# Performance work log

Measured on AMD Instinct MI355X. Metric: run time of the kernel, lower is better.

Reference implementation:

```python
import jax, jax.numpy as jnp
import numpy as np

INV_TEMP = 10.0

def pairwise_distance(x, y):
    # squared L2 distance: [b,n,c],[b,m,c] -> [b,n,m]
    x2 = jnp.sum(x * x, axis=-1, keepdims=True)          # [b,n,1]
    y2 = jnp.sum(y * y, axis=-1)[:, None, :]             # [b,1,m]
    xy = jnp.einsum('bnc,bmc->bnm', x, y)                # [b,n,m]
    return x2 + y2 - 2.0 * xy

def setup_inputs() -> dict:
    key = jax.random.key(0)
    k1, k2, k3 = jax.random.split(key, 3)
    b, n, m, c = 4, 4096, 4096, 32
    x_f = jax.random.normal(k1, (b, n, c), dtype=jnp.float32)
    y_f = jax.random.normal(k2, (b, m, c), dtype=jnp.float32)
    y_c = jax.random.normal(k3, (b, m, 3), dtype=jnp.float32)
    temp_inv = jnp.ones((1,), dtype=jnp.float32) * INV_TEMP
    return {"x_f": x_f, "y_f": y_f, "y_c": y_c, "temp_inv": temp_inv}

def reference(x_f, y_f, y_c, temp_inv):
    # corr_type='soft', st=True (straight-through)
    dist = pairwise_distance(x_f, y_f)                   # [b,n,m]
    y_soft = jax.nn.softmax(-dist * temp_inv[0], axis=2) # [b,n,m]
    index = jnp.argmax(y_soft, axis=2)                   # [b,n]
    y_hard = jax.nn.one_hot(index, y_soft.shape[2], dtype=y_soft.dtype)
    ret = y_hard - jax.lax.stop_gradient(y_soft) + y_soft
    x_corr = jnp.matmul(ret, y_c)                        # [b,n,3]
    return x_corr
```

## Files before the change

kernel.cpp:

```cpp
#include <hip/hip_runtime.h>

#define B 4
#define N 4096
#define M 4096
#define C 32
#define BN (B * N)
#define MS 16

typedef short bf16x8 __attribute__((ext_vector_type(8)));
typedef float f32x4  __attribute__((ext_vector_type(4)));
typedef unsigned int u32x4 __attribute__((ext_vector_type(4)));

#define WS_WI ((size_t)MS * BN * 4)
#define WS_YH (WS_WI * 2)
#define WS_YM (WS_YH + (size_t)B * M * C * 2)
#define WS_YL (WS_YM + (size_t)B * M * C * 2)
#define WS_Y2 (WS_YL + (size_t)B * M * C * 2)

__device__ __forceinline__ float bf16lo(unsigned int u) { return __uint_as_float(u << 16); }
__device__ __forceinline__ float bf16hi(unsigned int u) { return __uint_as_float(u & 0xffff0000u); }

__device__ __forceinline__ void split3(const float f[8], bf16x8& h, bf16x8& m, bf16x8& l) {
    u32x4 hw, mw, lw;
    #pragma unroll
    for (int p = 0; p < 4; ++p) {
        const float f0 = f[2*p], f1 = f[2*p+1];
        const unsigned int h0 = __float_as_uint(f0) & 0xffff0000u;
        const unsigned int h1 = __float_as_uint(f1) & 0xffff0000u;
        hw[p] = h1 | (h0 >> 16);
        const float r0 = f0 - __uint_as_float(h0);
        const float r1 = f1 - __uint_as_float(h1);
        const unsigned int m0 = __float_as_uint(r0) & 0xffff0000u;
        const unsigned int m1 = __float_as_uint(r1) & 0xffff0000u;
        mw[p] = m1 | (m0 >> 16);
        const float s0 = r0 - __uint_as_float(m0);
        const float s1 = r1 - __uint_as_float(m1);
        lw[p] = (__float_as_uint(s1) & 0xffff0000u) | (__float_as_uint(s0) >> 16);
    }
    h = __builtin_bit_cast(bf16x8, hw);
    m = __builtin_bit_cast(bf16x8, mw);
    l = __builtin_bit_cast(bf16x8, lw);
}

__global__ __launch_bounds__(256)
void y_prepass(const void* __restrict__ yptr, const unsigned short* __restrict__ tptr,
               void* __restrict__ ws) {
    if (tptr[0] == 0x4120) return;
    unsigned short* yh = (unsigned short*)((char*)ws + WS_YH);
    unsigned short* ym = (unsigned short*)((char*)ws + WS_YM);
    unsigned short* yl = (unsigned short*)((char*)ws + WS_YL);
    float*          y2 = (float*)((char*)ws + WS_Y2);

    const int gid = blockIdx.x * 256 + threadIdx.x;
    const int row = gid >> 2;
    const int seg = gid & 3;
    const float* p = (const float*)yptr + (size_t)row * C + seg * 8;
    float4 v0 = *(const float4*)p;
    float4 v1 = *(const float4*)(p + 4);
    const float f[8] = {v0.x, v0.y, v0.z, v0.w, v1.x, v1.y, v1.z, v1.w};

    bf16x8 h, m, l;
    split3(f, h, m, l);
    const size_t o = (size_t)row * C + seg * 8;
    *(bf16x8*)(yh + o) = h;
    *(bf16x8*)(ym + o) = m;
    *(bf16x8*)(yl + o) = l;

    float s = 0.f;
    #pragma unroll
    for (int k = 0; k < 8; ++k) s = fmaf(f[k], f[k], s);
    s += __shfl_xor(s, 1, 64);
    s += __shfl_xor(s, 2, 64);
    if (seg == 0) y2[row] = -0.5f * s;
}

__global__ __launch_bounds__(256, 4)
void nn_main(const void* __restrict__ xptr, const void* __restrict__ yptr,
             const unsigned short* __restrict__ tptr, void* __restrict__ ws) {
    float* wD = (float*)ws;
    int*   wI = (int*)((char*)ws + WS_WI);
    const bool is_bf16 = (tptr[0] == 0x4120);

    __shared__ float y2s[256];

    const int tid  = threadIdx.x;
    const int lane = tid & 63;
    const int wv   = tid >> 6;
    const int col  = lane & 15;
    const int quad = lane >> 4;
    const int bi   = blockIdx.x;
    const int ms   = bi & 15;
    const int nb   = (bi >> 4) & 31;
    const int b    = bi >> 9;
    const int n_base = nb * 128 + wv * 32;
    const int m0   = ms * 256;

    float bD[2][4];
    int   bI[2][4];
    #pragma unroll
    for (int t = 0; t < 2; ++t)
        #pragma unroll
        for (int r = 0; r < 4; ++r) { bD[t][r] = -__builtin_inff(); bI[t][r] = 0; }

    const size_t boff = (size_t)col * C + quad * 8;

    if (is_bf16) {
        const unsigned short* yp = (const unsigned short*)yptr;
        const unsigned short* xp = (const unsigned short*)xptr;

        if (tid < 256) {
            const int r = tid;
            const uint4* p = (const uint4*)(yp + ((size_t)b * M + m0 + r) * C);
            float s = 0.f;
            #pragma unroll
            for (int i = 0; i < 4; ++i) {
                uint4 v = p[i];
                float f;
                f = bf16lo(v.x); s = fmaf(f, f, s); f = bf16hi(v.x); s = fmaf(f, f, s);
                f = bf16lo(v.y); s = fmaf(f, f, s); f = bf16hi(v.y); s = fmaf(f, f, s);
                f = bf16lo(v.z); s = fmaf(f, f, s); f = bf16hi(v.z); s = fmaf(f, f, s);
                f = bf16lo(v.w); s = fmaf(f, f, s); f = bf16hi(v.w); s = fmaf(f, f, s);
            }
            y2s[r] = -0.5f * s;
        }

        bf16x8 af[2];
        #pragma unroll
        for (int t = 0; t < 2; ++t)
            af[t] = *(const bf16x8*)(xp + ((size_t)b * N + n_base + t * 16 + col) * C + quad * 8);

        __syncthreads();

        const unsigned short* yb = yp + ((size_t)b * M + m0) * C;
        bf16x8 bfr = *(const bf16x8*)(yb + boff);
        for (int mt = 0; mt < 16; ++mt) {
            bf16x8 bnx = bfr;
            if (mt < 15) bnx = *(const bf16x8*)(yb + boff + (size_t)(mt + 1) * (16 * C));
            const float y2c  = y2s[mt * 16 + col];
            const int   mcur = m0 + mt * 16 + col;
            #pragma unroll
            for (int t = 0; t < 2; ++t) {
                f32x4 acc = {y2c, y2c, y2c, y2c};
                acc = __builtin_amdgcn_mfma_f32_16x16x32_bf16(af[t], bfr, acc, 0, 0, 0);
                #pragma unroll
                for (int r = 0; r < 4; ++r)
                    if (acc[r] > bD[t][r]) { bD[t][r] = acc[r]; bI[t][r] = mcur; }
            }
            bfr = bnx;
        }
    } else {
        const unsigned short* yh = (const unsigned short*)((char*)ws + WS_YH) + ((size_t)b * M + m0) * C;
        const unsigned short* ym = (const unsigned short*)((char*)ws + WS_YM) + ((size_t)b * M + m0) * C;
        const unsigned short* yl = (const unsigned short*)((char*)ws + WS_YL) + ((size_t)b * M + m0) * C;
        const float*         y2g = (const float*)((char*)ws + WS_Y2) + (size_t)b * M + m0;

        if (tid < 256) y2s[tid] = y2g[tid];

        const float* xp = (const float*)xptr;
        bf16x8 ah[2], am[2], al[2];
        #pragma unroll
        for (int t = 0; t < 2; ++t) {
            const float* xr = xp + ((size_t)b * N + n_base + t * 16 + col) * C + quad * 8;
            float4 v0 = *(const float4*)xr;
            float4 v1 = *(const float4*)(xr + 4);
            const float xf[8] = {v0.x, v0.y, v0.z, v0.w, v1.x, v1.y, v1.z, v1.w};
            split3(xf, ah[t], am[t], al[t]);
        }

        __syncthreads();

        bf16x8 bh  = *(const bf16x8*)(yh + boff);
        bf16x8 bmi = *(const bf16x8*)(ym + boff);
        bf16x8 bl  = *(const bf16x8*)(yl + boff);
        for (int mt = 0; mt < 16; ++mt) {
            bf16x8 nh = bh, nm = bmi, nl = bl;
            if (mt < 15) {
                const size_t no = boff + (size_t)(mt + 1) * (16 * C);
                nh = *(const bf16x8*)(yh + no);
                nm = *(const bf16x8*)(ym + no);
                nl = *(const bf16x8*)(yl + no);
            }
            const float y2c  = y2s[mt * 16 + col];
            const int   mcur = m0 + mt * 16 + col;
            #pragma unroll
            for (int t = 0; t < 2; ++t) {
                f32x4 acc = {y2c, y2c, y2c, y2c};
                acc = __builtin_amdgcn_mfma_f32_16x16x32_bf16(am[t], bmi, acc, 0, 0, 0);
                acc = __builtin_amdgcn_mfma_f32_16x16x32_bf16(ah[t], bl,  acc, 0, 0, 0);
                acc = __builtin_amdgcn_mfma_f32_16x16x32_bf16(al[t], bh,  acc, 0, 0, 0);
                acc = __builtin_amdgcn_mfma_f32_16x16x32_bf16(ah[t], bmi, acc, 0, 0, 0);
                acc = __builtin_amdgcn_mfma_f32_16x16x32_bf16(am[t], bh,  acc, 0, 0, 0);
                acc = __builtin_amdgcn_mfma_f32_16x16x32_bf16(ah[t], bh,  acc, 0, 0, 0);
                #pragma unroll
                for (int r = 0; r < 4; ++r)
                    if (acc[r] > bD[t][r]) { bD[t][r] = acc[r]; bI[t][r] = mcur; }
            }
            bh = nh; bmi = nm; bl = nl;
        }
    }

    #pragma unroll
    for (int mask = 1; mask < 16; mask <<= 1) {
        #pragma unroll
        for (int t = 0; t < 2; ++t)
            #pragma unroll
            for (int r = 0; r < 4; ++r) {
                float oD = __shfl_xor(bD[t][r], mask, 64);
                int   oI = __shfl_xor(bI[t][r], mask, 64);
                if (oD > bD[t][r] || (oD == bD[t][r] && oI < bI[t][r])) {
                    bD[t][r] = oD; bI[t][r] = oI;
                }
            }
    }

    if (col == 0) {
        #pragma unroll
        for (int t = 0; t < 2; ++t)
            #pragma unroll
            for (int r = 0; r < 4; ++r) {
                const int n = n_base + t * 16 + quad * 4 + r;
                const size_t g = ((size_t)b * N + n) * MS + ms;
                wD[g] = bD[t][r];
                wI[g] = bI[t][r];
            }
    }
}

__global__ __launch_bounds__(256)
void nn_combine(const float* __restrict__ wD, const int* __restrict__ wI,
                const void* __restrict__ ycptr,
                const unsigned short* __restrict__ tptr,
                void* __restrict__ outptr) {
    const bool is_bf16 = (tptr[0] == 0x4120);
    const int tid  = threadIdx.x;
    const int lane = tid & 63;
    const int wv   = tid >> 6;
    const int s    = lane & 15;
    const int row  = blockIdx.x * 16 + wv * 4 + (lane >> 4);

    float k  = wD[(size_t)row * MS + s];
    int   ix = wI[(size_t)row * MS + s];
    #pragma unroll
    for (int mask = 1; mask < 16; mask <<= 1) {
        float ok = __shfl_xor(k, mask, 64);
        int   oi = __shfl_xor(ix, mask, 64);
        if (ok > k || (ok == k && oi < ix)) { k = ok; ix = oi; }
    }

    if (s == 0) {
        const int b = row >> 12;
        const size_t src = ((size_t)b * M + ix) * 3;
        if (is_bf16) {
            const unsigned short* yc = (const unsigned short*)ycptr;
            unsigned short* o = (unsigned short*)outptr;
            o[row*3+0] = yc[src+0];
            o[row*3+1] = yc[src+1];
            o[row*3+2] = yc[src+2];
        } else {
            const float* yc = (const float*)ycptr;
            float* o = (float*)outptr;
            o[row*3+0] = yc[src+0];
            o[row*3+1] = yc[src+1];
            o[row*3+2] = yc[src+2];
        }
    }
}

extern "C" void kernel_launch(void* const* d_in, const int* in_sizes, int n_in,
                              void* d_out, int out_size, void* d_ws, size_t ws_size,
                              hipStream_t stream) {
    const void* x  = d_in[0];
    const void* y  = d_in[1];
    const void* yc = d_in[2];
    const unsigned short* t = (const unsigned short*)d_in[3];

    float* wD = (float*)d_ws;
    int*   wI = (int*)((char*)d_ws + WS_WI);

    y_prepass<<<256, 256, 0, stream>>>(y, t, d_ws);
    nn_main<<<2048, 256, 0, stream>>>(x, y, t, d_ws);
    nn_combine<<<1024, 256, 0, stream>>>(wD, wI, yc, t, d_out);
}
```

Measured before the change: 99.86 us.

## Stage split y tiles in LDS and double rows per wave

The prepass now writes the three bf16 split planes of y in a chunk-contiguous layout, so each block can bulk-copy its 256-row tile (48KB) into shared memory and read B fragments from LDS instead of global memory. Each wave now handles 64 query rows instead of 32, so the grid is halved and every loaded y fragment feeds twice as many MFMAs. The partial-result workspace is transposed to slice-major order and the combine kernel's reduction is changed to match. The cost is more LDS and registers per block, with launch bounds lowered to 3 blocks per CU, which reduces occupancy.

```diff
diff --git a/kernel.cpp b/kernel.cpp
--- a/kernel.cpp
+++ b/kernel.cpp
@@ -12,10 +12,8 @@
 typedef unsigned int u32x4 __attribute__((ext_vector_type(4)));
 
 #define WS_WI ((size_t)MS * BN * 4)
-#define WS_YH (WS_WI * 2)
-#define WS_YM (WS_YH + (size_t)B * M * C * 2)
-#define WS_YL (WS_YM + (size_t)B * M * C * 2)
-#define WS_Y2 (WS_YL + (size_t)B * M * C * 2)
+#define WS_YP (WS_WI * 2)
+#define WS_Y2 (WS_YP + (size_t)B * M * C * 3 * 2)
 
 __device__ __forceinline__ float bf16lo(unsigned int u) { return __uint_as_float(u << 16); }
 __device__ __forceinline__ float bf16hi(unsigned int u) { return __uint_as_float(u & 0xffff0000u); }
@@ -46,25 +44,27 @@
 void y_prepass(const void* __restrict__ yptr, const unsigned short* __restrict__ tptr,
                void* __restrict__ ws) {
     if (tptr[0] == 0x4120) return;
-    unsigned short* yh = (unsigned short*)((char*)ws + WS_YH);
-    unsigned short* ym = (unsigned short*)((char*)ws + WS_YM);
-    unsigned short* yl = (unsigned short*)((char*)ws + WS_YL);
+    unsigned short* yp = (unsigned short*)((char*)ws + WS_YP);
     float*          y2 = (float*)((char*)ws + WS_Y2);
 
     const int gid = blockIdx.x * 256 + threadIdx.x;
     const int row = gid >> 2;
     const int seg = gid & 3;
+    const int b   = row >> 12;
+    const int m   = row & 4095;
+    const int chunk = m >> 8;
+    const int mr    = m & 255;
     const float* p = (const float*)yptr + (size_t)row * C + seg * 8;
     float4 v0 = *(const float4*)p;
     float4 v1 = *(const float4*)(p + 4);
     const float f[8] = {v0.x, v0.y, v0.z, v0.w, v1.x, v1.y, v1.z, v1.w};
 
-    bf16x8 h, m, l;
-    split3(f, h, m, l);
-    const size_t o = (size_t)row * C + seg * 8;
-    *(bf16x8*)(yh + o) = h;
-    *(bf16x8*)(ym + o) = m;
-    *(bf16x8*)(yl + o) = l;
+    bf16x8 h, m_, l;
+    split3(f, h, m_, l);
+    const size_t base = (size_t)((b * 16 + chunk) * 3) * 8192 + mr * 32 + seg * 8;
+    *(bf16x8*)(yp + base)            = h;
+    *(bf16x8*)(yp + base + 8192)     = m_;
+    *(bf16x8*)(yp + base + 16384)    = l;
 
     float s = 0.f;
     #pragma unroll
@@ -74,13 +74,14 @@
     if (seg == 0) y2[row] = -0.5f * s;
 }
 
-__global__ __launch_bounds__(256, 4)
+__global__ __launch_bounds__(256, 3)
 void nn_main(const void* __restrict__ xptr, const void* __restrict__ yptr,
              const unsigned short* __restrict__ tptr, void* __restrict__ ws) {
     float* wD = (float*)ws;
     int*   wI = (int*)((char*)ws + WS_WI);
     const bool is_bf16 = (tptr[0] == 0x4120);
 
+    __shared__ uint4 bpl[3072];
     __shared__ float y2s[256];
 
     const int tid  = threadIdx.x;
@@ -90,25 +91,23 @@
     const int quad = lane >> 4;
     const int bi   = blockIdx.x;
     const int ms   = bi & 15;
-    const int nb   = (bi >> 4) & 31;
-    const int b    = bi >> 9;
-    const int n_base = nb * 128 + wv * 32;
+    const int nb   = (bi >> 4) & 15;
+    const int b    = bi >> 8;
+    const int n_base = nb * 256 + wv * 64;
     const int m0   = ms * 256;
 
-    float bD[2][4];
-    int   bI[2][4];
-    #pragma unroll
-    for (int t = 0; t < 2; ++t)
+    float bD[4][4];
+    int   bI[4][4];
+    #pragma unroll
+    for (int t = 0; t < 4; ++t)
         #pragma unroll
         for (int r = 0; r < 4; ++r) { bD[t][r] = -__builtin_inff(); bI[t][r] = 0; }
-
-    const size_t boff = (size_t)col * C + quad * 8;
 
     if (is_bf16) {
         const unsigned short* yp = (const unsigned short*)yptr;
         const unsigned short* xp = (const unsigned short*)xptr;
 
-        if (tid < 256) {
+        {
             const int r = tid;
             const uint4* p = (const uint4*)(yp + ((size_t)b * M + m0 + r) * C);
             float s = 0.f;
@@ -124,14 +123,15 @@
             y2s[r] = -0.5f * s;
         }
 
-        bf16x8 af[2];
-        #pragma unroll
-        for (int t = 0; t < 2; ++t)
+        bf16x8 af[4];
+        #pragma unroll
+        for (int t = 0; t < 4; ++t)
             af[t] = *(const bf16x8*)(xp + ((size_t)b * N + n_base + t * 16 + col) * C + quad * 8);
 
         __syncthreads();
 
         const unsigned short* yb = yp + ((size_t)b * M + m0) * C;
+        const size_t boff = (size_t)col * C + quad * 8;
         bf16x8 bfr = *(const bf16x8*)(yb + boff);
         for (int mt = 0; mt < 16; ++mt) {
             bf16x8 bnx = bfr;
@@ -139,7 +139,7 @@
             const float y2c  = y2s[mt * 16 + col];
             const int   mcur = m0 + mt * 16 + col;
             #pragma unroll
-            for (int t = 0; t < 2; ++t) {
+            for (int t = 0; t < 4; ++t) {
                 f32x4 acc = {y2c, y2c, y2c, y2c};
                 acc = __builtin_amdgcn_mfma_f32_16x16x32_bf16(af[t], bfr, acc, 0, 0, 0);
                 #pragma unroll
@@ -149,17 +149,17 @@
             bfr = bnx;
         }
     } else {
-        const unsigned short* yh = (const unsigned short*)((char*)ws + WS_YH) + ((size_t)b * M + m0) * C;
-        const unsigned short* ym = (const unsigned short*)((char*)ws + WS_YM) + ((size_t)b * M + m0) * C;
-        const unsigned short* yl = (const unsigned short*)((char*)ws + WS_YL) + ((size_t)b * M + m0) * C;
-        const float*         y2g = (const float*)((char*)ws + WS_Y2) + (size_t)b * M + m0;
-
-        if (tid < 256) y2s[tid] = y2g[tid];
+        const uint4* src = (const uint4*)((char*)ws + WS_YP + (size_t)((b * 16 + ms) * 3) * 16384);
+        const float* y2g = (const float*)((char*)ws + WS_Y2) + (size_t)b * M + m0;
+
+        #pragma unroll
+        for (int i = 0; i < 12; ++i) bpl[tid + i * 256] = src[tid + i * 256];
+        y2s[tid] = y2g[tid];
 
         const float* xp = (const float*)xptr;
-        bf16x8 ah[2], am[2], al[2];
-        #pragma unroll
-        for (int t = 0; t < 2; ++t) {
+        bf16x8 ah[4], am[4], al[4];
+        #pragma unroll
+        for (int t = 0; t < 4; ++t) {
             const float* xr = xp + ((size_t)b * N + n_base + t * 16 + col) * C + quad * 8;
             float4 v0 = *(const float4*)xr;
             float4 v1 = *(const float4*)(xr + 4);
@@ -169,21 +169,24 @@
 
         __syncthreads();
 
-        bf16x8 bh  = *(const bf16x8*)(yh + boff);
-        bf16x8 bmi = *(const bf16x8*)(ym + boff);
-        bf16x8 bl  = *(const bf16x8*)(yl + boff);
+        const unsigned short* lds = (const unsigned short*)bpl;
+        const int fo = col * 32 + quad * 8;
+
+        bf16x8 bh  = *(const bf16x8*)(lds + fo);
+        bf16x8 bmi = *(const bf16x8*)(lds + 8192 + fo);
+        bf16x8 bl  = *(const bf16x8*)(lds + 16384 + fo);
         for (int mt = 0; mt < 16; ++mt) {
             bf16x8 nh = bh, nm = bmi, nl = bl;
             if (mt < 15) {
-                const size_t no = boff + (size_t)(mt + 1) * (16 * C);
-                nh = *(const bf16x8*)(yh + no);
-                nm = *(const bf16x8*)(ym + no);
-                nl = *(const bf16x8*)(yl + no);
+                const int no = fo + (mt + 1) * (16 * 32);
+                nh = *(const bf16x8*)(lds + no);
+                nm = *(const bf16x8*)(lds + 8192 + no);
+                nl = *(const bf16x8*)(lds + 16384 + no);
             }
             const float y2c  = y2s[mt * 16 + col];
             const int   mcur = m0 + mt * 16 + col;
             #pragma unroll
-            for (int t = 0; t < 2; ++t) {
+            for (int t = 0; t < 4; ++t) {
                 f32x4 acc = {y2c, y2c, y2c, y2c};
                 acc = __builtin_amdgcn_mfma_f32_16x16x32_bf16(am[t], bmi, acc, 0, 0, 0);
                 acc = __builtin_amdgcn_mfma_f32_16x16x32_bf16(ah[t], bl,  acc, 0, 0, 0);
@@ -202,7 +205,7 @@
     #pragma unroll
     for (int mask = 1; mask < 16; mask <<= 1) {
         #pragma unroll
-        for (int t = 0; t < 2; ++t)
+        for (int t = 0; t < 4; ++t)
             #pragma unroll
             for (int r = 0; r < 4; ++r) {
                 float oD = __shfl_xor(bD[t][r], mask, 64);
@@ -215,11 +218,11 @@
 
     if (col == 0) {
         #pragma unroll
-        for (int t = 0; t < 2; ++t)
+        for (int t = 0; t < 4; ++t)
             #pragma unroll
             for (int r = 0; r < 4; ++r) {
                 const int n = n_base + t * 16 + quad * 4 + r;
-                const size_t g = ((size_t)b * N + n) * MS + ms;
+                const size_t g = (size_t)ms * BN + (size_t)b * N + n;
                 wD[g] = bD[t][r];
                 wI[g] = bI[t][r];
             }
@@ -235,13 +238,14 @@
     const int tid  = threadIdx.x;
     const int lane = tid & 63;
     const int wv   = tid >> 6;
-    const int s    = lane & 15;
-    const int row  = blockIdx.x * 16 + wv * 4 + (lane >> 4);
-
-    float k  = wD[(size_t)row * MS + s];
-    int   ix = wI[(size_t)row * MS + s];
-    #pragma unroll
-    for (int mask = 1; mask < 16; mask <<= 1) {
+    const int s    = lane >> 2;
+    const int ro   = lane & 3;
+    const int row  = blockIdx.x * 16 + wv * 4 + ro;
+
+    float k  = wD[(size_t)s * BN + row];
+    int   ix = wI[(size_t)s * BN + row];
+    #pragma unroll
+    for (int mask = 4; mask < 64; mask <<= 1) {
         float ok = __shfl_xor(k, mask, 64);
         int   oi = __shfl_xor(ix, mask, 64);
         if (ok > k || (ok == k && oi < ix)) { k = ok; ix = oi; }
@@ -278,6 +282,6 @@
     int*   wI = (int*)((char*)d_ws + WS_WI);
 
     y_prepass<<<256, 256, 0, stream>>>(y, t, d_ws);
-    nn_main<<<2048, 256, 0, stream>>>(x, y, t, d_ws);
+    nn_main<<<1024, 256, 0, stream>>>(x, y, t, d_ws);
     nn_combine<<<1024, 256, 0, stream>>>(wD, wI, yc, t, d_out);
 }
```

Measured after the change: 94.69 us. -5.2%, faster.
